# Performance work log

Measured on AMD Instinct MI355X. Metric: run time of the kernel, lower is better.

The kernel has to match this reference:

```python
import jax, jax.numpy as jnp
import numpy as np

N_NODES = 8192
N_EDGES = 65536
IN_DIM = 768
HIDDEN = 4096
N_CLASSES = 16


def setup_inputs() -> dict:
    key = jax.random.key(0)
    k1, k2, k3, k4 = jax.random.split(key, 4)
    x = jax.random.normal(k1, (N_NODES, IN_DIM), dtype=jnp.float32)
    edge_index = jax.random.randint(k2, (2, N_EDGES), 0, N_NODES, dtype=jnp.int64)
    # Glorot-ish init scale
    W1 = jax.random.normal(k3, (IN_DIM, HIDDEN), dtype=jnp.float32) * (1.0 / np.sqrt(IN_DIM))
    b1 = jnp.zeros((HIDDEN,), dtype=jnp.float32)
    W2 = jax.random.normal(k4, (HIDDEN, N_CLASSES), dtype=jnp.float32) * (1.0 / np.sqrt(HIDDEN))
    b2 = jnp.zeros((N_CLASSES,), dtype=jnp.float32)
    return {"x": x, "edge_index": edge_index, "W1": W1, "b1": b1, "W2": W2, "b2": b2}


def reference(x, edge_index, W1, b1, W2, b2):
    # GCNConv (PyG defaults): add self-loops, symmetric deg^-1/2 normalization,
    # transform-then-aggregate, plus bias. Then ReLU -> (dropout=identity at
    # inference) -> Linear -> log_softmax.
    N = x.shape[0]
    loops = jnp.arange(N, dtype=edge_index.dtype)
    src = jnp.concatenate([edge_index[0], loops])  # [E+N]
    dst = jnp.concatenate([edge_index[1], loops])  # [E+N]

    h = x @ W1  # [N, HIDDEN] dense GEMM

    deg = jax.ops.segment_sum(jnp.ones_like(dst, dtype=h.dtype), dst, num_segments=N)
    dinv = jnp.where(deg > 0, jax.lax.rsqrt(jnp.maximum(deg, 1e-12)), 0.0)
    norm = dinv[src] * dinv[dst]  # [E+N]

    agg = jax.ops.segment_sum(h[src] * norm[:, None], dst, num_segments=N)  # [N, HIDDEN]
    h = jax.nn.relu(agg + b1)

    logits = h @ W2 + b2  # [N, N_CLASSES]
    return jax.nn.log_softmax(logits, axis=1)
```

## Files before the change

kernel.cpp:

```cpp
#include <hip/hip_runtime.h>

#define N_NODES   8192
#define N_EDGES   65536
#define IN_DIM    768
#define HIDDEN    4096
#define N_CLASSES 16
#define SLOTS     64

typedef unsigned short ushort_t;
typedef __attribute__((ext_vector_type(8))) short bf16x8;
typedef __attribute__((ext_vector_type(4))) float f32x4;

__device__ __forceinline__ ushort_t f2bf(float f) {
    union { float f; unsigned i; } v; v.f = f;
    unsigned r = v.i + 0x7FFFu + ((v.i >> 16) & 1u);
    return (ushort_t)(r >> 16);
}
__device__ __forceinline__ float bf2f(ushort_t u) {
    union { unsigned i; float f; } v; v.i = ((unsigned)u) << 16; return v.f;
}

#define GLD_LDS16(gp, lp) \
    __builtin_amdgcn_global_load_lds((const __attribute__((address_space(1))) void*)(gp), \
                                     (__attribute__((address_space(3))) void*)(lp), 16, 0, 0)

__device__ __forceinline__ int esrc(const int* ei, int f32mode, int e) {
    return f32mode ? ei[e] : ei[2 * e];
}
__device__ __forceinline__ int edst(const int* ei, int f32mode, int e) {
    return f32mode ? ei[N_EDGES + e] : ei[2 * N_EDGES + 2 * e];
}

__global__ __launch_bounds__(256) void phase1(const float* __restrict__ x,
                                              ushort_t* __restrict__ xbf,
                                              const float* __restrict__ W2,
                                              ushort_t* __restrict__ W2T,
                                              const int* __restrict__ ei,
                                              int* __restrict__ cnt,
                                              int* __restrict__ slots,
                                              int* __restrict__ flag) {
    int b = blockIdx.x, t = threadIdx.x;
    if (b < 16) {
        __shared__ ushort_t ld[16 * 257];
        int k0 = b * 256;
        const float4* src = (const float4*)(W2 + (long)(k0 + t) * N_CLASSES);
        #pragma unroll
        for (int j = 0; j < 4; j++) {
            float4 v = src[j];
            ld[(j * 4 + 0) * 257 + t] = f2bf(v.x);
            ld[(j * 4 + 1) * 257 + t] = f2bf(v.y);
            ld[(j * 4 + 2) * 257 + t] = f2bf(v.z);
            ld[(j * 4 + 3) * 257 + t] = f2bf(v.w);
        }
        __syncthreads();
        #pragma unroll
        for (int c = 0; c < 16; c++)
            W2T[c * HIDDEN + k0 + t] = ld[c * 257 + t];
    } else if (b < 1552) {
        long i = (long)(b - 16) * 1024 + t;
        #pragma unroll
        for (int p = 0; p < 4; p++) {
            float4 v = ((const float4*)x)[i + p * 256];
            ushort4 r = { f2bf(v.x), f2bf(v.y), f2bf(v.z), f2bf(v.w) };
            ((ushort4*)xbf)[i + p * 256] = r;
        }
    } else {
        __shared__ int sv[256];
        int v = 0;
        for (int e = t; e < 4096; e += 256) v |= ei[2 * e + 1];
        sv[t] = v;
        __syncthreads();
        for (int off = 128; off > 0; off >>= 1) {
            if (t < off) sv[t] |= sv[t + off];
            __syncthreads();
        }
        int f = (sv[0] != 0) ? 1 : 0;
        if (b == 1552 && t == 0) *flag = f;
        int e = (b - 1552) * 256 + t;
        int s = esrc(ei, f, e), d = edst(ei, f, e);
        int p = atomicAdd(&cnt[d], 1);
        if (p < SLOTS) slots[d * SLOTS + p] = s;
    }
}

__global__ __launch_bounds__(256) void phase2(const float* __restrict__ W1,
                                              ushort_t* __restrict__ W1T,
                                              const ushort_t* __restrict__ xbf,
                                              const int* __restrict__ cnt,
                                              const int* __restrict__ slots,
                                              const int* __restrict__ ei,
                                              const int* __restrict__ flag,
                                              ushort_t* __restrict__ xagg) {
    int b = blockIdx.x, t = threadIdx.x;
    if (b < 3072) {
        __shared__ ushort_t tile[32][33];
        int n0 = (b & 127) * 32, k0 = (b >> 7) * 32;
        int tx = t & 31, ty = t >> 5;
        #pragma unroll
        for (int j = 0; j < 4; j++) {
            int k = ty * 4 + j;
            tile[k][tx] = f2bf(W1[(k0 + k) * HIDDEN + n0 + tx]);
        }
        __syncthreads();
        #pragma unroll
        for (int j = 0; j < 4; j++) {
            int n = ty * 4 + j;
            W1T[(n0 + n) * IN_DIM + k0 + tx] = tile[tx][n];
        }
        return;
    }
    if (t >= 192) return;
    int w = t >> 6, l = t & 63;
    int d = b - 3072;
    int fo = w * 256 + l * 4;
    int cd = cnt[d];
    float wd = rsqrtf((float)(cd + 1));
    ushort4 sv = *(const ushort4*)(xbf + (long)d * IN_DIM + fo);
    float a0 = wd * bf2f(sv.x), a1 = wd * bf2f(sv.y);
    float a2 = wd * bf2f(sv.z), a3 = wd * bf2f(sv.w);

    if (cd <= SLOTS) {
        const int* sl = slots + d * SLOTS;
        int j = 0;
        for (; j + 4 <= cd; j += 4) {
            int s0 = sl[j], s1 = sl[j + 1], s2 = sl[j + 2], s3 = sl[j + 3];
            float w0 = rsqrtf((float)(cnt[s0] + 1));
            float w1 = rsqrtf((float)(cnt[s1] + 1));
            float w2 = rsqrtf((float)(cnt[s2] + 1));
            float w3 = rsqrtf((float)(cnt[s3] + 1));
            ushort4 v0 = *(const ushort4*)(xbf + (long)s0 * IN_DIM + fo);
            ushort4 v1 = *(const ushort4*)(xbf + (long)s1 * IN_DIM + fo);
            ushort4 v2 = *(const ushort4*)(xbf + (long)s2 * IN_DIM + fo);
            ushort4 v3 = *(const ushort4*)(xbf + (long)s3 * IN_DIM + fo);
            a0 = fmaf(w0, bf2f(v0.x), a0); a1 = fmaf(w0, bf2f(v0.y), a1);
            a2 = fmaf(w0, bf2f(v0.z), a2); a3 = fmaf(w0, bf2f(v0.w), a3);
            a0 = fmaf(w1, bf2f(v1.x), a0); a1 = fmaf(w1, bf2f(v1.y), a1);
            a2 = fmaf(w1, bf2f(v1.z), a2); a3 = fmaf(w1, bf2f(v1.w), a3);
            a0 = fmaf(w2, bf2f(v2.x), a0); a1 = fmaf(w2, bf2f(v2.y), a1);
            a2 = fmaf(w2, bf2f(v2.z), a2); a3 = fmaf(w2, bf2f(v2.w), a3);
            a0 = fmaf(w3, bf2f(v3.x), a0); a1 = fmaf(w3, bf2f(v3.y), a1);
            a2 = fmaf(w3, bf2f(v3.z), a2); a3 = fmaf(w3, bf2f(v3.w), a3);
        }
        for (; j < cd; j++) {
            int s = sl[j];
            float ws = rsqrtf((float)(cnt[s] + 1));
            ushort4 v = *(const ushort4*)(xbf + (long)s * IN_DIM + fo);
            a0 = fmaf(ws, bf2f(v.x), a0); a1 = fmaf(ws, bf2f(v.y), a1);
            a2 = fmaf(ws, bf2f(v.z), a2); a3 = fmaf(ws, bf2f(v.w), a3);
        }
    } else {
        int f = *flag;
        for (int e = 0; e < N_EDGES; e++) {
            if (edst(ei, f, e) == d) {
                int s = esrc(ei, f, e);
                float ws = rsqrtf((float)(cnt[s] + 1));
                ushort4 v = *(const ushort4*)(xbf + (long)s * IN_DIM + fo);
                a0 = fmaf(ws, bf2f(v.x), a0); a1 = fmaf(ws, bf2f(v.y), a1);
                a2 = fmaf(ws, bf2f(v.z), a2); a3 = fmaf(ws, bf2f(v.w), a3);
            }
        }
    }
    ushort4 r = { f2bf(a0 * wd), f2bf(a1 * wd), f2bf(a2 * wd), f2bf(a3 * wd) };
    *(ushort4*)(xagg + (long)d * IN_DIM + fo) = r;
}

__global__ __launch_bounds__(256) void gemm1_fused(const ushort_t* __restrict__ A,
                                                   const ushort_t* __restrict__ Bt,
                                                   const float* __restrict__ b1,
                                                   const ushort_t* __restrict__ W2T,
                                                   float* __restrict__ part) {
    __shared__ char smem[32768];
    ushort_t* ldsA = (ushort_t*)smem;
    ushort_t* ldsB = (ushort_t*)(smem + 16384);
    int bx = blockIdx.x & 31;
    int by = blockIdx.x >> 5;
    int m0 = by * 128, n0 = bx * 128;
    int t = threadIdx.x;
    int w = t >> 6, l = t & 63;
    int wm = w & 1, wn = w >> 1;
    int q = l >> 4, lm = l & 15;

    f32x4 acc[4][4] = {};

    int offA[4], offB[4];
    #pragma unroll
    for (int mt = 0; mt < 4; mt++) {
        int m = wm * 64 + mt * 16 + lm;
        offA[mt] = m * 32 + (q ^ ((m >> 1) & 3)) * 8;
    }
    #pragma unroll
    for (int nt = 0; nt < 4; nt++) {
        int n = wn * 64 + nt * 16 + lm;
        offB[nt] = n * 32 + (q ^ ((n >> 1) & 3)) * 8;
    }

    const ushort_t* pA[2][2];
    const ushort_t* pB[2][2];
    #pragma unroll
    for (int i = 0; i < 2; i++) {
        int L = i * 256 + t;
        int row = L >> 2;
        int cg = (L & 3) ^ ((row >> 1) & 3);
        const ushort_t* a0 = A + (long)(m0 + row) * IN_DIM + cg * 8;
        const ushort_t* b0 = Bt + (long)(n0 + row) * IN_DIM + cg * 8;
        pA[0][i] = a0;      pA[1][i] = a0 + 32;
        pB[0][i] = b0;      pB[1][i] = b0 + 32;
    }

    for (int it = 0; it < IN_DIM / 64; it++) {
        __syncthreads();
        #pragma unroll
        for (int i = 0; i < 2; i++) {
            GLD_LDS16(pA[0][i], ldsA + (i * 256 + w * 64) * 8);
            GLD_LDS16(pB[0][i], ldsB + (i * 256 + w * 64) * 8);
            GLD_LDS16(pA[1][i], ldsA + 4096 + (i * 256 + w * 64) * 8);
            GLD_LDS16(pB[1][i], ldsB + 4096 + (i * 256 + w * 64) * 8);
        }
        #pragma unroll
        for (int i = 0; i < 2; i++) {
            pA[0][i] += 64; pA[1][i] += 64;
            pB[0][i] += 64; pB[1][i] += 64;
        }
        __syncthreads();

        #pragma unroll
        for (int j = 0; j < 2; j++) {
            bf16x8 af[4], bfr[4];
            #pragma unroll
            for (int mt = 0; mt < 4; mt++)
                af[mt] = *(const bf16x8*)(ldsA + j * 4096 + offA[mt]);
            #pragma unroll
            for (int nt = 0; nt < 4; nt++)
                bfr[nt] = *(const bf16x8*)(ldsB + j * 4096 + offB[nt]);
            #pragma unroll
            for (int mt = 0; mt < 4; mt++)
                #pragma unroll
                for (int nt = 0; nt < 4; nt++)
                    acc[mt][nt] = __builtin_amdgcn_mfma_f32_16x16x32_bf16(af[mt], bfr[nt], acc[mt][nt], 0, 0, 0);
        }
    }

    __syncthreads();
    const int RP = 80;
    ushort_t* myhl = (ushort_t*)smem + w * 32 * RP;

    float bias[4];
    #pragma unroll
    for (int nt = 0; nt < 4; nt++) bias[nt] = b1[n0 + wn * 64 + nt * 16 + lm];

    bf16x8 bf2[2];
    #pragma unroll
    for (int kk = 0; kk < 2; kk++)
        bf2[kk] = *(const bf16x8*)(W2T + (long)lm * HIDDEN + n0 + wn * 64 + kk * 32 + q * 8);

    f32x4 acc2[4] = {};
    #pragma unroll
    for (int h = 0; h < 2; h++) {
        #pragma unroll
        for (int mt2 = 0; mt2 < 2; mt2++) {
            int mt = h * 2 + mt2;
            #pragma unroll
            for (int nt = 0; nt < 4; nt++) {
                #pragma unroll
                for (int r = 0; r < 4; r++) {
                    float v = acc[mt][nt][r] + bias[nt];
                    v = v > 0.0f ? v : 0.0f;
                    myhl[(mt2 * 16 + q * 4 + r) * RP + nt * 16 + lm] = f2bf(v);
                }
            }
        }
        #pragma unroll
        for (int kk = 0; kk < 2; kk++)
            #pragma unroll
            for (int mt2 = 0; mt2 < 2; mt2++) {
                bf16x8 a2 = *(const bf16x8*)(myhl + (mt2 * 16 + lm) * RP + kk * 32 + q * 8);
                acc2[h * 2 + mt2] = __builtin_amdgcn_mfma_f32_16x16x32_bf16(a2, bf2[kk], acc2[h * 2 + mt2], 0, 0, 0);
            }
    }

    float* psum = (float*)smem;
    __syncthreads();
    if (wn == 1) {
        #pragma unroll
        for (int mt = 0; mt < 4; mt++)
            #pragma unroll
            for (int r = 0; r < 4; r++)
                psum[(wm * 64 + mt * 16 + q * 4 + r) * 17 + lm] = acc2[mt][r];
    }
    __syncthreads();
    if (wn == 0) {
        float* pslab = part + ((long)bx * N_NODES + m0 + wm * 64) * N_CLASSES;
        #pragma unroll
        for (int mt = 0; mt < 4; mt++)
            #pragma unroll
            for (int r = 0; r < 4; r++) {
                float v = acc2[mt][r] + psum[(wm * 64 + mt * 16 + q * 4 + r) * 17 + lm];
                pslab[(mt * 16 + q * 4 + r) * N_CLASSES + lm] = v;
            }
    }
}

__global__ __launch_bounds__(256) void reduce_softmax(const float* __restrict__ part,
                                                      const float* __restrict__ b2,
                                                      float* __restrict__ out) {
    int t = threadIdx.x;
    int row = blockIdx.x * 16 + (t >> 4);
    int cls = t & 15;
    float v = b2[cls];
    #pragma unroll
    for (int s = 0; s < 32; s++)
        v += part[((long)s * N_NODES + row) * N_CLASSES + cls];
    float mx = v;
    #pragma unroll
    for (int off = 1; off < 16; off <<= 1)
        mx = fmaxf(mx, __shfl_xor(mx, off, 64));
    float e = __expf(v - mx);
    float sm = e;
    #pragma unroll
    for (int off = 1; off < 16; off <<= 1)
        sm += __shfl_xor(sm, off, 64);
    out[(long)row * N_CLASSES + cls] = v - mx - __logf(sm);
}


extern "C" void kernel_launch(void* const* d_in, const int* in_sizes, int n_in,
                              void* d_out, int out_size, void* d_ws, size_t ws_size,
                              hipStream_t stream) {
    const float* x  = (const float*)d_in[0];
    const int*   ei = (const int*)d_in[1];
    const float* W1 = (const float*)d_in[2];
    const float* b1 = (const float*)d_in[3];
    const float* W2 = (const float*)d_in[4];
    const float* b2 = (const float*)d_in[5];
    float* out = (float*)d_out;
    char* ws = (char*)d_ws;

    float*    part  = (float*)(ws);
    ushort_t* xagg  = (ushort_t*)(ws + 16777216);
    ushort_t* xbf   = (ushort_t*)(ws + 29360128);
    ushort_t* W1T   = (ushort_t*)(ws + 41943040);
    ushort_t* W2T   = (ushort_t*)(ws + 48234496);
    int*      cnt   = (int*)(ws + 48365568);
    int*      slots = (int*)(ws + 48398336);
    int*      flag  = (int*)(ws + 50495488);

    hipMemsetAsync(cnt, 0, 32768, stream);
    phase1<<<1808, 256, 0, stream>>>(x, xbf, W2, W2T, ei, cnt, slots, flag);
    phase2<<<11264, 256, 0, stream>>>(W1, W1T, xbf, cnt, slots, ei, flag, xagg);
    gemm1_fused<<<(N_NODES / 128) * (HIDDEN / 128), 256, 0, stream>>>(xagg, W1T, b1, W2T, part);
    reduce_softmax<<<N_NODES / 16, 256, 0, stream>>>(part, b2, out);
}
```

Measured before the change: 175.4 us.

## Rewrite fused GEMM as 256x256 tile, 8-wave, double-buffered pipelined kernel

```diff
diff --git a/kernel.cpp b/kernel.cpp
--- a/kernel.cpp
+++ b/kernel.cpp
@@ -6,6 +6,7 @@
 #define HIDDEN    4096
 #define N_CLASSES 16
 #define SLOTS     64
+#define NSLAB     16
 
 typedef unsigned short ushort_t;
 typedef __attribute__((ext_vector_type(8))) short bf16x8;
@@ -164,140 +165,173 @@
     *(ushort4*)(xagg + (long)d * IN_DIM + fo) = r;
 }
 
-__global__ __launch_bounds__(256) void gemm1_fused(const ushort_t* __restrict__ A,
-                                                   const ushort_t* __restrict__ Bt,
-                                                   const float* __restrict__ b1,
-                                                   const ushort_t* __restrict__ W2T,
-                                                   float* __restrict__ part) {
-    __shared__ char smem[32768];
-    ushort_t* ldsA = (ushort_t*)smem;
-    ushort_t* ldsB = (ushort_t*)(smem + 16384);
-    int bx = blockIdx.x & 31;
-    int by = blockIdx.x >> 5;
-    int m0 = by * 128, n0 = bx * 128;
+#define FENCE() asm volatile("" ::: "memory")
+#define BAR()  do { FENCE(); __builtin_amdgcn_s_barrier(); FENCE(); } while (0)
+#define VMCNT(n) asm volatile("s_waitcnt vmcnt(" #n ")" ::: "memory")
+#define LGKM0()  asm volatile("s_waitcnt lgkmcnt(0)" ::: "memory")
+#define PRIO(x)  __builtin_amdgcn_s_setprio(x)
+
+__global__ __launch_bounds__(512, 2) void gemm1_fused(const ushort_t* __restrict__ A,
+                                                      const ushort_t* __restrict__ Bt,
+                                                      const float* __restrict__ b1,
+                                                      const ushort_t* __restrict__ W2T,
+                                                      float* __restrict__ part) {
+    __shared__ ushort_t lds[65536];
+    ushort_t* ldsA = lds;
+    ushort_t* ldsB = lds + 32768;
+
     int t = threadIdx.x;
     int w = t >> 6, l = t & 63;
-    int wm = w & 1, wn = w >> 1;
+    int wm = w & 3, wn = w >> 2;
     int q = l >> 4, lm = l & 15;
-
-    f32x4 acc[4][4] = {};
-
-    int offA[4], offB[4];
-    #pragma unroll
-    for (int mt = 0; mt < 4; mt++) {
-        int m = wm * 64 + mt * 16 + lm;
-        offA[mt] = m * 32 + (q ^ ((m >> 1) & 3)) * 8;
-    }
-    #pragma unroll
-    for (int nt = 0; nt < 4; nt++) {
-        int n = wn * 64 + nt * 16 + lm;
-        offB[nt] = n * 32 + (q ^ ((n >> 1) & 3)) * 8;
-    }
-
-    const ushort_t* pA[2][2];
-    const ushort_t* pB[2][2];
-    #pragma unroll
-    for (int i = 0; i < 2; i++) {
-        int L = i * 256 + t;
-        int row = L >> 2;
-        int cg = (L & 3) ^ ((row >> 1) & 3);
-        const ushort_t* a0 = A + (long)(m0 + row) * IN_DIM + cg * 8;
-        const ushort_t* b0 = Bt + (long)(n0 + row) * IN_DIM + cg * 8;
-        pA[0][i] = a0;      pA[1][i] = a0 + 32;
-        pB[0][i] = b0;      pB[1][i] = b0 + 32;
-    }
-
-    for (int it = 0; it < IN_DIM / 64; it++) {
-        __syncthreads();
-        #pragma unroll
-        for (int i = 0; i < 2; i++) {
-            GLD_LDS16(pA[0][i], ldsA + (i * 256 + w * 64) * 8);
-            GLD_LDS16(pB[0][i], ldsB + (i * 256 + w * 64) * 8);
-            GLD_LDS16(pA[1][i], ldsA + 4096 + (i * 256 + w * 64) * 8);
-            GLD_LDS16(pB[1][i], ldsB + 4096 + (i * 256 + w * 64) * 8);
-        }
-        #pragma unroll
-        for (int i = 0; i < 2; i++) {
-            pA[0][i] += 64; pA[1][i] += 64;
-            pB[0][i] += 64; pB[1][i] += 64;
-        }
-        __syncthreads();
-
-        #pragma unroll
-        for (int j = 0; j < 2; j++) {
-            bf16x8 af[4], bfr[4];
-            #pragma unroll
-            for (int mt = 0; mt < 4; mt++)
-                af[mt] = *(const bf16x8*)(ldsA + j * 4096 + offA[mt]);
-            #pragma unroll
-            for (int nt = 0; nt < 4; nt++)
-                bfr[nt] = *(const bf16x8*)(ldsB + j * 4096 + offB[nt]);
-            #pragma unroll
-            for (int mt = 0; mt < 4; mt++)
-                #pragma unroll
-                for (int nt = 0; nt < 4; nt++)
-                    acc[mt][nt] = __builtin_amdgcn_mfma_f32_16x16x32_bf16(af[mt], bfr[nt], acc[mt][nt], 0, 0, 0);
-        }
-    }
+    int bx = blockIdx.x & 15, by = blockIdx.x >> 4;
+    int m0 = by * 256, n0 = bx * 256;
+
+    int srow = t >> 3;
+    int sg = (t & 7) ^ (srow & 7);
+    const ushort_t* aS = A  + (long)(m0 + srow) * IN_DIM + sg * 8;
+    const ushort_t* bS = Bt + (long)(n0 + srow) * IN_DIM + sg * 8;
+
+#define STAGE_A(B_, h, ko) do { \
+    GLD_LDS16(aS + (h) * 128 * IN_DIM + (ko),              ldsA + (B_) * 16384 + (h) * 8192 + w * 512); \
+    GLD_LDS16(aS + ((h) * 128 + 64) * IN_DIM + (ko),       ldsA + (B_) * 16384 + (h) * 8192 + 4096 + w * 512); \
+} while (0)
+#define STAGE_B(B_, h, ko) do { \
+    GLD_LDS16(bS + (h) * 128 * IN_DIM + (ko),              ldsB + (B_) * 16384 + (h) * 8192 + w * 512); \
+    GLD_LDS16(bS + ((h) * 128 + 64) * IN_DIM + (ko),       ldsB + (B_) * 16384 + (h) * 8192 + 4096 + w * 512); \
+} while (0)
+#define LDA(dst, qm, B_) do { \
+    const ushort_t* p_ = ldsA + (B_) * 16384 + (wm * 64 + (qm) * 32 + lm) * 64; \
+    int x0_ = ((q) ^ (lm & 7)) * 8, x1_ = ((4 + q) ^ (lm & 7)) * 8; \
+    dst[0][0] = *(const bf16x8*)(p_ + x0_);        dst[0][1] = *(const bf16x8*)(p_ + x1_); \
+    dst[1][0] = *(const bf16x8*)(p_ + 1024 + x0_); dst[1][1] = *(const bf16x8*)(p_ + 1024 + x1_); \
+} while (0)
+#define LDB(dst, qn, B_) do { \
+    const ushort_t* p_ = ldsB + (B_) * 16384 + (wn * 128 + (qn) * 64 + lm) * 64; \
+    int x0_ = ((q) ^ (lm & 7)) * 8, x1_ = ((4 + q) ^ (lm & 7)) * 8; \
+    dst[0][0] = *(const bf16x8*)(p_ + x0_);        dst[0][1] = *(const bf16x8*)(p_ + x1_); \
+    dst[1][0] = *(const bf16x8*)(p_ + 1024 + x0_); dst[1][1] = *(const bf16x8*)(p_ + 1024 + x1_); \
+    dst[2][0] = *(const bf16x8*)(p_ + 2048 + x0_); dst[2][1] = *(const bf16x8*)(p_ + 2048 + x1_); \
+    dst[3][0] = *(const bf16x8*)(p_ + 3072 + x0_); dst[3][1] = *(const bf16x8*)(p_ + 3072 + x1_); \
+} while (0)
+#define MFMAQ(qm, qn, a_, b_) do { \
+    _Pragma("unroll") for (int j_ = 0; j_ < 2; j_++) \
+    _Pragma("unroll") for (int nt_ = 0; nt_ < 4; nt_++) \
+    _Pragma("unroll") for (int mt_ = 0; mt_ < 2; mt_++) \
+        acc[(qm) * 2 + mt_][(qn) * 4 + nt_] = __builtin_amdgcn_mfma_f32_16x16x32_bf16( \
+            a_[mt_][j_], b_[nt_][j_], acc[(qm) * 2 + mt_][(qn) * 4 + nt_], 0, 0, 0); \
+} while (0)
+
+    int kA = 0, kB = 0;
+    STAGE_A(0, 0, kA); STAGE_A(0, 1, kA); kA += 64;
+    STAGE_B(0, 0, kB); STAGE_B(0, 1, kB); kB += 64;
+    STAGE_A(1, 0, kA); STAGE_A(1, 1, kA); kA += 64;
+
+    bf16x8 aq0[2][2], aq1[2][2], bq0[4][2], bq1[4][2];
+    f32x4 acc[4][8] = {};
+
+    VMCNT(4);
+    BAR();
+
+    #pragma unroll 1
+    for (int it = 0; it < 5; ++it) {
+        LDA(aq0, 0, 0); LDB(bq0, 0, 0); STAGE_B(1, 0, kB);
+        BAR(); LGKM0(); PRIO(1); MFMAQ(0, 0, aq0, bq0); PRIO(0); BAR();
+        LDA(aq1, 1, 0); STAGE_B(1, 1, kB); kB += 64;
+        BAR(); LGKM0(); PRIO(1); MFMAQ(1, 0, aq1, bq0); PRIO(0); BAR();
+        LDB(bq1, 1, 0); STAGE_A(0, 0, kA);
+        BAR(); LGKM0(); PRIO(1); MFMAQ(1, 1, aq1, bq1); PRIO(0); BAR();
+        STAGE_A(0, 1, kA); kA += 64;
+        VMCNT(4);
+        BAR(); PRIO(1); MFMAQ(0, 1, aq0, bq1); PRIO(0); BAR();
+        LDA(aq0, 0, 1); LDB(bq0, 0, 1); STAGE_B(0, 0, kB);
+        BAR(); LGKM0(); PRIO(1); MFMAQ(0, 0, aq0, bq0); PRIO(0); BAR();
+        LDA(aq1, 1, 1); STAGE_B(0, 1, kB); kB += 64;
+        BAR(); LGKM0(); PRIO(1); MFMAQ(1, 0, aq1, bq0); PRIO(0); BAR();
+        LDB(bq1, 1, 1); STAGE_A(1, 0, kA);
+        BAR(); LGKM0(); PRIO(1); MFMAQ(1, 1, aq1, bq1); PRIO(0); BAR();
+        STAGE_A(1, 1, kA); kA += 64;
+        VMCNT(4);
+        BAR(); PRIO(1); MFMAQ(0, 1, aq0, bq1); PRIO(0); BAR();
+    }
+    LDA(aq0, 0, 0); LDB(bq0, 0, 0); STAGE_B(1, 0, kB);
+    BAR(); LGKM0(); PRIO(1); MFMAQ(0, 0, aq0, bq0); PRIO(0); BAR();
+    LDA(aq1, 1, 0); STAGE_B(1, 1, kB);
+    BAR(); LGKM0(); PRIO(1); MFMAQ(1, 0, aq1, bq0); PRIO(0); BAR();
+    LDB(bq1, 1, 0);
+    BAR(); LGKM0(); PRIO(1); MFMAQ(1, 1, aq1, bq1); PRIO(0); BAR();
+    VMCNT(0);
+    BAR(); PRIO(1); MFMAQ(0, 1, aq0, bq1); PRIO(0); BAR();
+    LDA(aq0, 0, 1); LDB(bq0, 0, 1);
+    BAR(); LGKM0(); PRIO(1); MFMAQ(0, 0, aq0, bq0); PRIO(0); BAR();
+    LDA(aq1, 1, 1);
+    BAR(); LGKM0(); PRIO(1); MFMAQ(1, 0, aq1, bq0); PRIO(0); BAR();
+    LDB(bq1, 1, 1);
+    BAR(); LGKM0(); PRIO(1); MFMAQ(1, 1, aq1, bq1); PRIO(0); BAR();
+    PRIO(1); MFMAQ(0, 1, aq0, bq1); PRIO(0);
+
+    float bias[8];
+    #pragma unroll
+    for (int ng = 0; ng < 8; ng++) bias[ng] = b1[n0 + wn * 128 + ng * 16 + lm];
+    bf16x8 w2f[2][2];
+    #pragma unroll
+    for (int eh = 0; eh < 2; eh++)
+        #pragma unroll
+        for (int kk = 0; kk < 2; kk++)
+            w2f[eh][kk] = *(const bf16x8*)(W2T + (long)lm * HIDDEN + n0 + wn * 128 + eh * 64 + kk * 32 + q * 8);
 
     __syncthreads();
-    const int RP = 80;
-    ushort_t* myhl = (ushort_t*)smem + w * 32 * RP;
-
-    float bias[4];
-    #pragma unroll
-    for (int nt = 0; nt < 4; nt++) bias[nt] = b1[n0 + wn * 64 + nt * 16 + lm];
-
-    bf16x8 bf2[2];
-    #pragma unroll
-    for (int kk = 0; kk < 2; kk++)
-        bf2[kk] = *(const bf16x8*)(W2T + (long)lm * HIDDEN + n0 + wn * 64 + kk * 32 + q * 8);
-
+    ushort_t* slab = lds + w * 4096;
     f32x4 acc2[4] = {};
     #pragma unroll
-    for (int h = 0; h < 2; h++) {
-        #pragma unroll
-        for (int mt2 = 0; mt2 < 2; mt2++) {
-            int mt = h * 2 + mt2;
+    for (int eh = 0; eh < 2; eh++) {
+        #pragma unroll
+        for (int mg = 0; mg < 4; mg++)
             #pragma unroll
             for (int nt = 0; nt < 4; nt++) {
+                int gc = nt * 2 + (lm >> 3);
                 #pragma unroll
-                for (int r = 0; r < 4; r++) {
-                    float v = acc[mt][nt][r] + bias[nt];
+                for (int rr = 0; rr < 4; rr++) {
+                    int row = mg * 16 + q * 4 + rr;
+                    float v = acc[mg][eh * 4 + nt][rr] + bias[eh * 4 + nt];
                     v = v > 0.0f ? v : 0.0f;
-                    myhl[(mt2 * 16 + q * 4 + r) * RP + nt * 16 + lm] = f2bf(v);
+                    slab[row * 64 + ((gc ^ (row & 7)) * 8) + (lm & 7)] = f2bf(v);
                 }
             }
-        }
         #pragma unroll
         for (int kk = 0; kk < 2; kk++)
             #pragma unroll
-            for (int mt2 = 0; mt2 < 2; mt2++) {
-                bf16x8 a2 = *(const bf16x8*)(myhl + (mt2 * 16 + lm) * RP + kk * 32 + q * 8);
-                acc2[h * 2 + mt2] = __builtin_amdgcn_mfma_f32_16x16x32_bf16(a2, bf2[kk], acc2[h * 2 + mt2], 0, 0, 0);
+            for (int mt2 = 0; mt2 < 4; mt2++) {
+                bf16x8 a2 = *(const bf16x8*)(slab + (mt2 * 16 + lm) * 64 + (((kk * 4 + q) ^ (lm & 7)) * 8));
+                acc2[mt2] = __builtin_amdgcn_mfma_f32_16x16x32_bf16(a2, w2f[eh][kk], acc2[mt2], 0, 0, 0);
             }
     }
 
-    float* psum = (float*)smem;
     __syncthreads();
+    float* psum = (float*)lds;
     if (wn == 1) {
         #pragma unroll
-        for (int mt = 0; mt < 4; mt++)
+        for (int mt2 = 0; mt2 < 4; mt2++)
             #pragma unroll
-            for (int r = 0; r < 4; r++)
-                psum[(wm * 64 + mt * 16 + q * 4 + r) * 17 + lm] = acc2[mt][r];
+            for (int rr = 0; rr < 4; rr++)
+                psum[(wm * 64 + mt2 * 16 + q * 4 + rr) * 17 + lm] = acc2[mt2][rr];
     }
     __syncthreads();
     if (wn == 0) {
         float* pslab = part + ((long)bx * N_NODES + m0 + wm * 64) * N_CLASSES;
         #pragma unroll
-        for (int mt = 0; mt < 4; mt++)
+        for (int mt2 = 0; mt2 < 4; mt2++)
             #pragma unroll
-            for (int r = 0; r < 4; r++) {
-                float v = acc2[mt][r] + psum[(wm * 64 + mt * 16 + q * 4 + r) * 17 + lm];
-                pslab[(mt * 16 + q * 4 + r) * N_CLASSES + lm] = v;
+            for (int rr = 0; rr < 4; rr++) {
+                int row = mt2 * 16 + q * 4 + rr;
+                pslab[row * N_CLASSES + lm] = acc2[mt2][rr] + psum[(wm * 64 + row) * 17 + lm];
             }
     }
+#undef STAGE_A
+#undef STAGE_B
+#undef LDA
+#undef LDB
+#undef MFMAQ
 }
 
 __global__ __launch_bounds__(256) void reduce_softmax(const float* __restrict__ part,
@@ -308,7 +342,7 @@
     int cls = t & 15;
     float v = b2[cls];
     #pragma unroll
-    for (int s = 0; s < 32; s++)
+    for (int s = 0; s < NSLAB; s++)
         v += part[((long)s * N_NODES + row) * N_CLASSES + cls];
     float mx = v;
     #pragma unroll
@@ -347,6 +381,6 @@
     hipMemsetAsync(cnt, 0, 32768, stream);
     phase1<<<1808, 256, 0, stream>>>(x, xbf, W2, W2T, ei, cnt, slots, flag);
     phase2<<<11264, 256, 0, stream>>>(W1, W1T, xbf, cnt, slots, ei, flag, xagg);
-    gemm1_fused<<<(N_NODES / 128) * (HIDDEN / 128), 256, 0, stream>>>(xagg, W1T, b1, W2T, part);
+    gemm1_fused<<<(N_NODES / 256) * (HIDDEN / 256), 512, 0, stream>>>(xagg, W1T, b1, W2T, part);
     reduce_softmax<<<N_NODES / 16, 256, 0, stream>>>(part, b2, out);
 }
```

New measurement: 159.7 us, median of 2. 8.9% less time.
